# Optimization experiments

Hardware: AMD Instinct MI355X
Metric: run time of the kernel (lower is better)

Reference implementation:

```python
import jax, jax.numpy as jnp
import numpy as np

N_NODES = 17   # fixed by Linear(256, 17) + residual add
D = 512        # feature dim
H = 8          # number of attention heads


def setup_inputs() -> dict:
    key = jax.random.key(0)
    ks = jax.random.split(key, 8)
    return {
        "Xs": jax.random.normal(ks[0], (N_NODES, D), dtype=jnp.float32),
        "ROIs_b": jax.random.uniform(ks[1], (N_NODES, 3), dtype=jnp.float32),
        "adj": jnp.zeros((N_NODES, N_NODES), dtype=jnp.float32),  # unused in forward
        "FC": jax.random.normal(ks[2], (H, D, D), dtype=jnp.float32) * (1.414 / np.sqrt(D)),
        "W1": jax.random.normal(ks[3], (H, D + 3, 256), dtype=jnp.float32) * (1.0 / np.sqrt(D + 3)),
        "b1": jnp.zeros((H, 256), dtype=jnp.float32),
        "W2": jax.random.normal(ks[4], (H, 256, N_NODES), dtype=jnp.float32) * (1.0 / np.sqrt(256)),
        "b2": jnp.zeros((H, N_NODES), dtype=jnp.float32),
        "conv_w": jax.random.normal(ks[5], (H,), dtype=jnp.float32) * 0.3,
        "conv_b": jnp.zeros((1,), dtype=jnp.float32),
    }


def reference(Xs, ROIs_b, adj, FC, W1, b1, W2, b2, conv_w, conv_b):
    # All 8 heads batched over leading axis h (original launches them as
    # separate Python-level modules).
    # f_input = relu(Xs @ FC) per head: [H, N, D]
    f = jax.nn.relu(jnp.einsum('nd,hde->hne', Xs, FC))
    # concat coordinates: [H, N, D+3]
    coords = jnp.broadcast_to(ROIs_b[None], (f.shape[0], ROIs_b.shape[0], ROIs_b.shape[1]))
    cat = jnp.concatenate([f, coords], axis=-1)
    # 2-layer MLP: Linear(515,256) -> tanh -> Linear(256,17): [H, N, 17]
    hdn = jnp.tanh(jnp.einsum('hnc,hcm->hnm', cat, W1) + b1[:, None, :])
    att = jnp.einsum('hnm,hmk->hnk', hdn, W2) + b2[:, None, :]
    # permute(1,0) then softmax over dim=1 (the N axis): [H, 17, N]
    att = jax.nn.softmax(jnp.swapaxes(att, 1, 2), axis=-1)
    # weighted sum over nodes: [H, 17, D]
    h_prime = jnp.einsum('hkn,hnd->hkd', att, f)
    # Conv1d(8,1,1) over head axis + ReLU, then residual
    out = jax.nn.relu(jnp.einsum('h,hkd->kd', conv_w, h_prime) + conv_b[0])
    Xs_out = out + Xs  # [17, 512]
    # original returns a list of per-landmark views [1,512,1,1,1]; we return
    # the equivalent stacked array plus passthrough ROIs
    return Xs_out, ROIs_b
```

## Files before the change

### kernel.cpp

```cpp
#include <hip/hip_runtime.h>

#define NN 17
#define D  512
#define H  8
#define C1 515
#define M  256

#define NBLOCKS 128

#define XPAD 20
#define RSN  36
#define RSG  (NN * RSN)
#define SMEM_FL (32 * RSG)

#define CTR1(h)  ((h) * 32)
#define CTR2H(h) (256 + (h) * 32)
#define CTR2F    512

__device__ __forceinline__ void fma4(float4& a, float x, const float4& w) {
    a.x = fmaf(x, w.x, a.x); a.y = fmaf(x, w.y, a.y);
    a.z = fmaf(x, w.z, a.z); a.w = fmaf(x, w.w, a.w);
}

__device__ __forceinline__ void store_agent(float* p, float v) {
    __hip_atomic_store(p, v, __ATOMIC_RELAXED, __HIP_MEMORY_SCOPE_AGENT);
}

__device__ __forceinline__ unsigned ctr_add(unsigned* c) {
    return __hip_atomic_fetch_add(c, 1u, __ATOMIC_RELAXED, __HIP_MEMORY_SCOPE_AGENT);
}

__device__ __forceinline__ void arrive(unsigned* c) {
    asm volatile("s_waitcnt vmcnt(0)" ::: "memory");
    __syncthreads();
    if (threadIdx.x == 0) ctr_add(c);
}

__device__ __forceinline__ void wait_ge(unsigned* c, unsigned nb) {
    if (threadIdx.x == 0) {
        while (__hip_atomic_load(c, __ATOMIC_RELAXED, __HIP_MEMORY_SCOPE_AGENT) < nb) {
            __builtin_amdgcn_s_sleep(1);
        }
    }
    __syncthreads();
}

__global__ __launch_bounds__(256) void fused_all(
        const float* __restrict__ Xs,     const float* __restrict__ ROIs,
        const float* __restrict__ FC,     const float* __restrict__ W1,
        const float* __restrict__ b1,     const float* __restrict__ W2,
        const float* __restrict__ b2,     const float* __restrict__ conv_w,
        const float* __restrict__ conv_b, float* __restrict__ out,
        float* __restrict__ f,            float* __restrict__ hdn,
        unsigned int* __restrict__ ctrs) {
    const int b = blockIdx.x;
    const int t = threadIdx.x;
    const int tw = t & 7, cgr = t >> 3;
    __shared__ __align__(16) float sm[SMEM_FL];

    {
        const int et = b & 15, h1 = b >> 4;
        float4 wreg[16];
        const float4* fc4 = (const float4*)(FC + (size_t)h1 * D * D) + et * 8 + tw;
#pragma unroll
        for (int i = 0; i < 16; ++i) wreg[i] = fc4[(cgr + (i << 5)) << 7];
        for (int i = t; i < NN * D; i += 256) {
            const int n = i >> 9, d = i & 511;
            sm[d * XPAD + n] = Xs[i];
        }
        __syncthreads();
        float4 acc[NN];
#pragma unroll
        for (int n = 0; n < NN; ++n) acc[n] = make_float4(0.f, 0.f, 0.f, 0.f);
#pragma unroll
        for (int i = 0; i < 16; ++i) {
            const float4 w = wreg[i];
            const float* xr = sm + (cgr + (i << 5)) * XPAD;
#pragma unroll
            for (int n4 = 0; n4 < 4; ++n4) {
                const float4 x = *(const float4*)(xr + (n4 << 2));
                fma4(acc[n4 * 4 + 0], x.x, w);
                fma4(acc[n4 * 4 + 1], x.y, w);
                fma4(acc[n4 * 4 + 2], x.z, w);
                fma4(acc[n4 * 4 + 3], x.w, w);
            }
            fma4(acc[16], xr[16], w);
        }
        __syncthreads();
        float* rr = sm + cgr * RSG + tw * 4;
#pragma unroll
        for (int n = 0; n < NN; ++n) *(float4*)(rr + n * RSN) = acc[n];
        __syncthreads();
        for (int i = t; i < NN * 32; i += 256) {
            const int n = i >> 5, e = i & 31;
            float s = 0.f;
#pragma unroll 8
            for (int g = 0; g < 32; ++g) s += sm[g * RSG + n * RSN + e];
            store_agent(&f[((h1 * NN + n) << 9) + (et << 5) + e], fmaxf(s, 0.f));
        }
        arrive(ctrs + CTR1(h1));
    }
    if (b >= H * 8) return;

    {
        const int mt = b & 7, h2 = b >> 3;
        float4 w1r[17];
        const float4* w4 = (const float4*)(W1 + (size_t)h2 * C1 * M) + mt * 8 + tw;
#pragma unroll
        for (int i = 0; i < 16; ++i) w1r[i] = w4[(cgr + (i << 5)) << 6];
        w1r[16] = (cgr < 3) ? w4[(D + cgr) << 6] : make_float4(0.f, 0.f, 0.f, 0.f);
        __builtin_amdgcn_sched_barrier(0);
        wait_ge(ctrs + CTR1(h2), 16);
        for (int i = t; i < NN * D; i += 256) {
            const int n = i >> 9, d = i & 511;
            sm[d * XPAD + n] = f[((size_t)(h2 * NN) << 9) + i];
        }
        if (t < NN * 3) {
            const int n = t / 3, cc = t % 3;
            sm[(D + cc) * XPAD + n] = ROIs[t];
        }
        __syncthreads();
        float4 acc[NN];
#pragma unroll
        for (int n = 0; n < NN; ++n) acc[n] = make_float4(0.f, 0.f, 0.f, 0.f);
#pragma unroll
        for (int i = 0; i < 16; ++i) {
            const float4 w = w1r[i];
            const float* xr = sm + (cgr + (i << 5)) * XPAD;
#pragma unroll
            for (int n4 = 0; n4 < 4; ++n4) {
                const float4 x = *(const float4*)(xr + (n4 << 2));
                fma4(acc[n4 * 4 + 0], x.x, w);
                fma4(acc[n4 * 4 + 1], x.y, w);
                fma4(acc[n4 * 4 + 2], x.z, w);
                fma4(acc[n4 * 4 + 3], x.w, w);
            }
            fma4(acc[16], xr[16], w);
        }
        if (cgr < 3) {
            const float4 w = w1r[16];
            const float* xr = sm + (D + cgr) * XPAD;
#pragma unroll
            for (int n4 = 0; n4 < 4; ++n4) {
                const float4 x = *(const float4*)(xr + (n4 << 2));
                fma4(acc[n4 * 4 + 0], x.x, w);
                fma4(acc[n4 * 4 + 1], x.y, w);
                fma4(acc[n4 * 4 + 2], x.z, w);
                fma4(acc[n4 * 4 + 3], x.w, w);
            }
            fma4(acc[16], xr[16], w);
        }
        __syncthreads();
        float* rr = sm + cgr * RSG + tw * 4;
#pragma unroll
        for (int n = 0; n < NN; ++n) *(float4*)(rr + n * RSN) = acc[n];
        __syncthreads();
        for (int i = t; i < NN * 32; i += 256) {
            const int n = i >> 5, m = i & 31;
            float s = b1[h2 * M + (mt << 5) + m];
#pragma unroll 8
            for (int g = 0; g < 32; ++g) s += sm[g * RSG + n * RSN + m];
            store_agent(&hdn[(h2 * NN + n) * M + (mt << 5) + m], tanhf(s));
        }
        asm volatile("s_waitcnt vmcnt(0)" ::: "memory");
        __syncthreads();
        if (t == 0) {
            if (ctr_add(ctrs + CTR2H(h2)) == 7u) ctr_add(ctrs + CTR2F);
        }
    }
    if (b >= NN) return;

    {
        const int k = b;
        float* swk = sm;
        float* sa  = sm + H * (M + 4);
        float* cwv = sm + H * (M + 4) + H * NN;
        for (int i = t; i < H * M; i += 256) {
            const int h = i >> 8, m = i & 255;
            swk[h * (M + 4) + m] = W2[(size_t)(h * M + m) * NN + k];
        }
        if (t < H) cwv[t] = conv_w[t];
        __builtin_amdgcn_sched_barrier(0);
        wait_ge(ctrs + CTR2F, 8);
        if (t < H * NN) {
            const int h = t / NN, n = t % NN;
            const float4* a4 = (const float4*)(hdn + (h * NN + n) * M);
            const float4* w4 = (const float4*)(swk + h * (M + 4));
            float acc = b2[h * NN + k];
#pragma unroll 8
            for (int m4 = 0; m4 < M / 4; ++m4) {
                const float4 av = a4[m4];
                const float4 wv = w4[m4];
                acc = fmaf(av.x, wv.x, acc); acc = fmaf(av.y, wv.y, acc);
                acc = fmaf(av.z, wv.z, acc); acc = fmaf(av.w, wv.w, acc);
            }
            sa[h * NN + n] = acc;
        }
        __syncthreads();
        if (t < H) {
            float mx = -1e30f;
#pragma unroll
            for (int n = 0; n < NN; ++n) mx = fmaxf(mx, sa[t * NN + n]);
            float e[NN];
            float s = 0.f;
#pragma unroll
            for (int n = 0; n < NN; ++n) { e[n] = __expf(sa[t * NN + n] - mx); s += e[n]; }
            const float inv = 1.f / s;
#pragma unroll
            for (int n = 0; n < NN; ++n) sa[t * NN + n] = e[n] * inv;
        }
        __syncthreads();
        const float cb = conv_b[0];
        float acc0 = 0.f, acc1 = 0.f;
        for (int h = 0; h < H; ++h) {
            float w0 = 0.f, w1 = 0.f;
#pragma unroll
            for (int n = 0; n < NN; ++n) {
                const float a = sa[h * NN + n];
                const float* fr = f + (size_t)((h * NN + n) << 9);
                w0 = fmaf(a, fr[t], w0);
                w1 = fmaf(a, fr[t + 256], w1);
            }
            acc0 = fmaf(cwv[h], w0, acc0);
            acc1 = fmaf(cwv[h], w1, acc1);
        }
        out[(k << 9) + t]       = fmaxf(acc0 + cb, 0.f) + Xs[(k << 9) + t];
        out[(k << 9) + t + 256] = fmaxf(acc1 + cb, 0.f) + Xs[(k << 9) + t + 256];
        if (k == 0 && t < NN * 3) out[NN * D + t] = ROIs[t];
    }
}

extern "C" void kernel_launch(void* const* d_in, const int* in_sizes, int n_in,
                              void* d_out, int out_size, void* d_ws, size_t ws_size,
                              hipStream_t stream) {
    const float* Xs     = (const float*)d_in[0];
    const float* ROIs   = (const float*)d_in[1];
    const float* FC     = (const float*)d_in[3];
    const float* W1     = (const float*)d_in[4];
    const float* b1     = (const float*)d_in[5];
    const float* W2     = (const float*)d_in[6];
    const float* b2     = (const float*)d_in[7];
    const float* conv_w = (const float*)d_in[8];
    const float* conv_b = (const float*)d_in[9];
    float* outp = (float*)d_out;

    float* fbuf   = (float*)d_ws;
    float* hdnbuf = fbuf + H * NN * D;

    unsigned int* ctrs = (unsigned int*)((char*)d_ws + (1u << 20));
    hipMemsetAsync(ctrs, 0, (512 + 32) * sizeof(unsigned int), stream);

    fused_all<<<NBLOCKS, 256, 0, stream>>>(Xs, ROIs, FC, W1, b1, W2, b2,
                                           conv_w, conv_b, outp, fbuf, hdnbuf,
                                           ctrs);
}
```

Measured before the change: 108.6 us.

## Split fused kernel into two launches, replacing stage-1 spin barrier with kernel boundary

Splits the persistent fused kernel into a first kernel computing relu(Xs@FC) and a second kernel running the MLP, softmax and conv stages. The first-stage atomic counters and spin-wait are replaced by the stream ordering between launches. This removes cross-block polling and atomic traffic, but adds a kernel launch gap. It also gives up overlapping the W1 register preload with stage-1 compute.

```diff
diff --git a/kernel.cpp b/kernel.cpp
--- a/kernel.cpp
+++ b/kernel.cpp
@@ -6,14 +6,11 @@
 #define C1 515
 #define M  256
 
-#define NBLOCKS 128
-
 #define XPAD 20
 #define RSN  36
 #define RSG  (NN * RSN)
 #define SMEM_FL (32 * RSG)
 
-#define CTR1(h)  ((h) * 32)
 #define CTR2H(h) (256 + (h) * 32)
 #define CTR2F    512
 
@@ -28,12 +25,6 @@
 
 __device__ __forceinline__ unsigned ctr_add(unsigned* c) {
     return __hip_atomic_fetch_add(c, 1u, __ATOMIC_RELAXED, __HIP_MEMORY_SCOPE_AGENT);
-}
-
-__device__ __forceinline__ void arrive(unsigned* c) {
-    asm volatile("s_waitcnt vmcnt(0)" ::: "memory");
-    __syncthreads();
-    if (threadIdx.x == 0) ctr_add(c);
 }
 
 __device__ __forceinline__ void wait_ge(unsigned* c, unsigned nb) {
@@ -45,63 +36,68 @@
     __syncthreads();
 }
 
-__global__ __launch_bounds__(256) void fused_all(
-        const float* __restrict__ Xs,     const float* __restrict__ ROIs,
-        const float* __restrict__ FC,     const float* __restrict__ W1,
-        const float* __restrict__ b1,     const float* __restrict__ W2,
-        const float* __restrict__ b2,     const float* __restrict__ conv_w,
-        const float* __restrict__ conv_b, float* __restrict__ out,
-        float* __restrict__ f,            float* __restrict__ hdn,
-        unsigned int* __restrict__ ctrs) {
-    const int b = blockIdx.x;
-    const int t = threadIdx.x;
+__global__ __launch_bounds__(256) void kA_f(const float* __restrict__ Xs,
+                                            const float* __restrict__ FC,
+                                            float* __restrict__ f) {
+    const int b = blockIdx.x, t = threadIdx.x;
+    const int tw = t & 7, cgr = t >> 3;
+    const int et = b & 15, h1 = b >> 4;
+    __shared__ __align__(16) float sm[SMEM_FL];
+    float4 wreg[16];
+    const float4* fc4 = (const float4*)(FC + (size_t)h1 * D * D) + et * 8 + tw;
+#pragma unroll
+    for (int i = 0; i < 16; ++i) wreg[i] = fc4[(cgr + (i << 5)) << 7];
+    for (int i = t; i < NN * D; i += 256) {
+        const int n = i >> 9, d = i & 511;
+        sm[d * XPAD + n] = Xs[i];
+    }
+    __syncthreads();
+    float4 acc[NN];
+#pragma unroll
+    for (int n = 0; n < NN; ++n) acc[n] = make_float4(0.f, 0.f, 0.f, 0.f);
+#pragma unroll
+    for (int i = 0; i < 16; ++i) {
+        const float4 w = wreg[i];
+        const float* xr = sm + (cgr + (i << 5)) * XPAD;
+#pragma unroll
+        for (int n4 = 0; n4 < 4; ++n4) {
+            const float4 x = *(const float4*)(xr + (n4 << 2));
+            fma4(acc[n4 * 4 + 0], x.x, w);
+            fma4(acc[n4 * 4 + 1], x.y, w);
+            fma4(acc[n4 * 4 + 2], x.z, w);
+            fma4(acc[n4 * 4 + 3], x.w, w);
+        }
+        fma4(acc[16], xr[16], w);
+    }
+    __syncthreads();
+    float* rr = sm + cgr * RSG + tw * 4;
+#pragma unroll
+    for (int n = 0; n < NN; ++n) *(float4*)(rr + n * RSN) = acc[n];
+    __syncthreads();
+    for (int i = t; i < NN * 32; i += 256) {
+        const int n = i >> 5, e = i & 31;
+        float s = 0.f;
+#pragma unroll 8
+        for (int g = 0; g < 32; ++g) s += sm[g * RSG + n * RSN + e];
+        f[((h1 * NN + n) << 9) + (et << 5) + e] = fmaxf(s, 0.f);
+    }
+}
+
+__global__ __launch_bounds__(256) void kB_23(const float* __restrict__ f,
+                                             const float* __restrict__ ROIs,
+                                             const float* __restrict__ W1,
+                                             const float* __restrict__ b1,
+                                             const float* __restrict__ W2,
+                                             const float* __restrict__ b2,
+                                             const float* __restrict__ conv_w,
+                                             const float* __restrict__ conv_b,
+                                             const float* __restrict__ Xs,
+                                             float* __restrict__ hdn,
+                                             float* __restrict__ out,
+                                             unsigned int* __restrict__ ctrs) {
+    const int b = blockIdx.x, t = threadIdx.x;
     const int tw = t & 7, cgr = t >> 3;
     __shared__ __align__(16) float sm[SMEM_FL];
-
-    {
-        const int et = b & 15, h1 = b >> 4;
-        float4 wreg[16];
-        const float4* fc4 = (const float4*)(FC + (size_t)h1 * D * D) + et * 8 + tw;
-#pragma unroll
-        for (int i = 0; i < 16; ++i) wreg[i] = fc4[(cgr + (i << 5)) << 7];
-        for (int i = t; i < NN * D; i += 256) {
-            const int n = i >> 9, d = i & 511;
-            sm[d * XPAD + n] = Xs[i];
-        }
-        __syncthreads();
-        float4 acc[NN];
-#pragma unroll
-        for (int n = 0; n < NN; ++n) acc[n] = make_float4(0.f, 0.f, 0.f, 0.f);
-#pragma unroll
-        for (int i = 0; i < 16; ++i) {
-            const float4 w = wreg[i];
-            const float* xr = sm + (cgr + (i << 5)) * XPAD;
-#pragma unroll
-            for (int n4 = 0; n4 < 4; ++n4) {
-                const float4 x = *(const float4*)(xr + (n4 << 2));
-                fma4(acc[n4 * 4 + 0], x.x, w);
-                fma4(acc[n4 * 4 + 1], x.y, w);
-                fma4(acc[n4 * 4 + 2], x.z, w);
-                fma4(acc[n4 * 4 + 3], x.w, w);
-            }
-            fma4(acc[16], xr[16], w);
-        }
-        __syncthreads();
-        float* rr = sm + cgr * RSG + tw * 4;
-#pragma unroll
-        for (int n = 0; n < NN; ++n) *(float4*)(rr + n * RSN) = acc[n];
-        __syncthreads();
-        for (int i = t; i < NN * 32; i += 256) {
-            const int n = i >> 5, e = i & 31;
-            float s = 0.f;
-#pragma unroll 8
-            for (int g = 0; g < 32; ++g) s += sm[g * RSG + n * RSN + e];
-            store_agent(&f[((h1 * NN + n) << 9) + (et << 5) + e], fmaxf(s, 0.f));
-        }
-        arrive(ctrs + CTR1(h1));
-    }
-    if (b >= H * 8) return;
-
     {
         const int mt = b & 7, h2 = b >> 3;
         float4 w1r[17];
@@ -109,8 +105,6 @@
 #pragma unroll
         for (int i = 0; i < 16; ++i) w1r[i] = w4[(cgr + (i << 5)) << 6];
         w1r[16] = (cgr < 3) ? w4[(D + cgr) << 6] : make_float4(0.f, 0.f, 0.f, 0.f);
-        __builtin_amdgcn_sched_barrier(0);
-        wait_ge(ctrs + CTR1(h2), 16);
         for (int i = t; i < NN * D; i += 256) {
             const int n = i >> 9, d = i & 511;
             sm[d * XPAD + n] = f[((size_t)(h2 * NN) << 9) + i];
@@ -250,7 +244,7 @@
     unsigned int* ctrs = (unsigned int*)((char*)d_ws + (1u << 20));
     hipMemsetAsync(ctrs, 0, (512 + 32) * sizeof(unsigned int), stream);
 
-    fused_all<<<NBLOCKS, 256, 0, stream>>>(Xs, ROIs, FC, W1, b1, W2, b2,
-                                           conv_w, conv_b, outp, fbuf, hdnbuf,
-                                           ctrs);
-}
+    kA_f <<<H * 16, 256, 0, stream>>>(Xs, FC, fbuf);
+    kB_23<<<H * 8,  256, 0, stream>>>(fbuf, ROIs, W1, b1, W2, b2,
+                                      conv_w, conv_b, Xs, hdnbuf, outp, ctrs);
+}
```

Result: no change. 109.6 us (+0.9%).
